# Performance work log

Hardware: AMD Instinct MI355X
Metric: run time of the kernel (lower is better)

## Reference

```python
import jax, jax.numpy as jnp
import numpy as np

N_NODES = 50000
N_EDGES = 800000
N_FEAT = 128
N_GRAPHS = 512
OUT_DIM = 128


def gcn_conv(x, W, b, src, dst, ew, n):
    """PyG GCNConv: h = x @ W; add self-loops (weight 1); symmetric norm
    D^-1/2 A D^-1/2 with edge weights; scatter-add messages src->dst; + bias."""
    h = x @ W  # [n, out]
    loop = jnp.arange(n)
    s = jnp.concatenate([src, loop])
    d = jnp.concatenate([dst, loop])
    w = jnp.concatenate([ew, jnp.ones((n,), x.dtype)])
    deg = jax.ops.segment_sum(w, d, num_segments=n)
    dinv = jnp.where(deg > 0, jax.lax.rsqrt(deg), 0.0)
    norm = dinv[s] * w * dinv[d]  # [E+n]
    out = jax.ops.segment_sum(h[s] * norm[:, None], d, num_segments=n)
    return out + b


def setup_inputs() -> dict:
    key = jax.random.key(0)
    ks = jax.random.split(key, 12)
    F = N_FEAT
    x = jax.random.normal(ks[0], (N_NODES, F), jnp.float32)
    edge_index = jax.random.randint(ks[1], (2, N_EDGES), 0, N_NODES, jnp.int64)
    edge_attr = jax.random.uniform(ks[2], (N_EDGES,), jnp.float32)
    # deterministic sorted graph assignment -> no empty graphs (avoids -inf in max pool)
    batch = (jnp.arange(N_NODES, dtype=jnp.int64) * N_GRAPHS) // N_NODES
    def lin(k, fi, fo):
        s = 1.0 / np.sqrt(fi)
        return jax.random.uniform(k, (fi, fo), jnp.float32, -s, s)
    return {
        "x": x, "edge_attr": edge_attr,
        "W1": lin(ks[3], F, F), "b1": jnp.zeros((F,), jnp.float32),
        "W2": lin(ks[4], F, 2 * F), "b2": jnp.zeros((2 * F,), jnp.float32),
        "W3": lin(ks[5], 2 * F, 4 * F), "b3": jnp.zeros((4 * F,), jnp.float32),
        "Wf1": lin(ks[6], 4 * F, 1024), "bf1": jnp.zeros((1024,), jnp.float32),
        "Wf2": lin(ks[7], 1024, OUT_DIM), "bf2": jnp.zeros((OUT_DIM,), jnp.float32),
        "edge_index": edge_index, "batch": batch,
    }


def reference(x, edge_attr, W1, b1, W2, b2, W3, b3, Wf1, bf1, Wf2, bf2,
              edge_index, batch):
    n = x.shape[0]
    src, dst = edge_index[0], edge_index[1]
    h = jax.nn.relu(gcn_conv(x, W1, b1, src, dst, edge_attr, n))
    h = jax.nn.relu(gcn_conv(h, W2, b2, src, dst, edge_attr, n))
    h = jax.nn.relu(gcn_conv(h, W3, b3, src, dst, edge_attr, n))
    # global max pool over nodes per graph
    g = jax.ops.segment_max(h, batch, num_segments=N_GRAPHS)  # [G, 4F]
    g = jax.nn.relu(g @ Wf1 + bf1)
    # dropout is identity in eval mode
    out = g @ Wf2 + bf2
    return out
```

## Files before the change

### kernel.cpp

```cpp
#include <hip/hip_runtime.h>

#define NNODES 50000
#define NEDGES 800000
#define NGRAPH 512
#define DCAP 64

typedef short bf16x8 __attribute__((ext_vector_type(8)));
typedef unsigned short u16x8 __attribute__((ext_vector_type(8)));
typedef float f32x4 __attribute__((ext_vector_type(4)));
typedef unsigned long long u64;

static __device__ __forceinline__ float b2f(unsigned short u) {
    return __uint_as_float(((unsigned)u) << 16);
}
static __device__ __forceinline__ unsigned short f2b(float f) {
    unsigned u = __float_as_uint(f);
    unsigned r = (u + 0x7fffu + ((u >> 16) & 1u)) >> 16;
    return (unsigned short)r;
}

static __device__ __forceinline__ void accum8(float (&acc)[8], float c, uint4 v) {
    unsigned w[4] = {v.x, v.y, v.z, v.w};
    #pragma unroll
    for (int i = 0; i < 4; ++i) {
        acc[2 * i]     += c * __uint_as_float(w[i] << 16);
        acc[2 * i + 1] += c * __uint_as_float(w[i] & 0xffff0000u);
    }
}

__global__ __launch_bounds__(256) void k_init(const float* __restrict__ W1, const float* __restrict__ W2,
                                              const float* __restrict__ W3, const float* __restrict__ Wf1,
                                              const float* __restrict__ Wf2,
                                              unsigned short* __restrict__ T1, unsigned short* __restrict__ T2,
                                              unsigned short* __restrict__ T3, unsigned short* __restrict__ Tf1,
                                              unsigned short* __restrict__ Tf2,
                                              u64* deg_cnt, int* gp) {
    int i = blockIdx.x * 256 + threadIdx.x;
    if (i < NNODES) deg_cnt[i] = (u64)(1u << 24);
    if (i < NGRAPH * 512) gp[i] = 0;

    const int b = blockIdx.x;
    if (b >= 204) return;
    const float* W; unsigned short* T; int K, N, t0;
    if (b < 4)        { W = W1;  T = T1;  K = 128;  N = 128;  t0 = 0;   }
    else if (b < 12)  { W = W2;  T = T2;  K = 128;  N = 256;  t0 = 4;   }
    else if (b < 44)  { W = W3;  T = T3;  K = 256;  N = 512;  t0 = 12;  }
    else if (b < 172) { W = Wf1; T = Tf1; K = 512;  N = 1024; t0 = 44;  }
    else              { W = Wf2; T = Tf2; K = 1024; N = 128;  t0 = 172; }
    const int tile = b - t0;
    const int ntn = N >> 6;
    const int k0 = (tile / ntn) * 64, n0 = (tile % ntn) * 64;
    __shared__ float sm[64][65];
    const int t = threadIdx.x;
    const int rr = t >> 6, cc = t & 63;
    #pragma unroll
    for (int r = 0; r < 16; ++r) {
        int kl = r * 4 + rr;
        sm[kl][cc] = W[(size_t)(k0 + kl) * N + n0 + cc];
    }
    __syncthreads();
    #pragma unroll
    for (int r = 0; r < 16; ++r) {
        int nl = r * 4 + rr;
        T[(size_t)(n0 + nl) * K + k0 + cc] = f2b(sm[cc][nl]);
    }
}

__global__ __launch_bounds__(256) void k_count(const int4* __restrict__ ei_s,
                                               const int4* __restrict__ ei_d,
                                               const float4* __restrict__ ew4,
                                               u64* deg_cnt,
                                               unsigned* __restrict__ edges) {
    int t = blockIdx.x * 256 + threadIdx.x;
    if (t >= NEDGES / 4) return;
    int4 ss = ei_s[t];
    int4 dd = ei_d[t];
    float4 ww = ew4[t];
    int s[4] = {ss.x, ss.y, ss.z, ss.w};
    int d[4] = {dd.x, dd.y, dd.z, dd.w};
    float w[4] = {ww.x, ww.y, ww.z, ww.w};
    int slot[4];
    #pragma unroll
    for (int u = 0; u < 4; ++u) {
        unsigned fixed = __float2uint_rn(w[u] * 16777216.0f);
        u64 old = atomicAdd(&deg_cnt[d[u]], ((u64)1 << 32) | fixed);
        slot[u] = (int)(old >> 32);
        if (slot[u] > DCAP - 1) slot[u] = DCAP - 1;
    }
    #pragma unroll
    for (int u = 0; u < 4; ++u)
        edges[((unsigned)d[u] << 6) | slot[u]] = ((unsigned)f2b(w[u]) << 16) | (unsigned)s[u];
}

__global__ void k_prep(const u64* __restrict__ deg_cnt, float* __restrict__ dinv) {
    int i = blockIdx.x * 256 + threadIdx.x;
    if (i < NNODES)
        dinv[i] = rsqrtf((float)(unsigned)(deg_cnt[i] & 0xffffffffull) * 5.9604645e-8f);
}

__global__ void k_cvt4(const float* __restrict__ X, const float* __restrict__ dinv,
                       unsigned short* __restrict__ Y, int n4) {
    int i = blockIdx.x * 256 + threadIdx.x;
    if (i < n4) {
        float4 v = ((const float4*)X)[i];
        float d = dinv[i >> 5];
        uint2 o;
        o.x = (unsigned)f2b(v.x * d) | ((unsigned)f2b(v.y * d) << 16);
        o.y = (unsigned)f2b(v.z * d) | ((unsigned)f2b(v.w * d) << 16);
        ((uint2*)Y)[i] = o;
    }
}

template <int F>
__global__ __launch_bounds__(256) void k_aggregate(const unsigned short* __restrict__ X,
                                                   const u64* __restrict__ deg_cnt,
                                                   const unsigned* __restrict__ edges,
                                                   const float* __restrict__ dinv,
                                                   unsigned short* __restrict__ Z) {
    constexpr int LPR = F / 8;
    constexpr int GRP = 64 / LPR;
    constexpr int STEP = GRP * 2;
    const int wave = threadIdx.x >> 6, lane = threadIdx.x & 63;
    const int node = blockIdx.x * 4 + wave;
    if (node >= NNODES) return;
    const int sub = lane & (LPR - 1);
    const int grp = lane / LPR;
    const int fo = sub * 8;
    const unsigned short* Xf = X + fo;
    const float di = dinv[node];
    const int cnt = (int)(deg_cnt[node] >> 32);
    const unsigned* erow = edges + ((unsigned)node << 6);

    const uint4 selfv = *(const uint4*)(Xf + (size_t)node * F);

    float acc[8] = {};

    const int e0 = grp;
    const int nb = (cnt + STEP - 1) / STEP;

    unsigned pa0 = 0, pb0 = 0, pa1 = 0, pb1 = 0;
    uint4 va0 = {}, vb0 = {};
    if (nb > 0) {
        int ea = e0, eb = e0 + GRP;
        pa0 = (ea < cnt) ? erow[ea] : 0u;
        pb0 = (eb < cnt) ? erow[eb] : 0u;
        va0 = *(const uint4*)(Xf + (size_t)(pa0 & 0xffffu) * F);
        vb0 = *(const uint4*)(Xf + (size_t)(pb0 & 0xffffu) * F);
        if (nb > 1) {
            int ea1 = e0 + STEP, eb1 = ea1 + GRP;
            pa1 = (ea1 < cnt) ? erow[ea1] : 0u;
            pb1 = (eb1 < cnt) ? erow[eb1] : 0u;
        }
    }
    for (int p = 0; p < nb; ++p) {
        uint4 va1 = {}, vb1 = {};
        unsigned pa2 = 0, pb2 = 0;
        if (p + 1 < nb) {
            va1 = *(const uint4*)(Xf + (size_t)(pa1 & 0xffffu) * F);
            vb1 = *(const uint4*)(Xf + (size_t)(pb1 & 0xffffu) * F);
            if (p + 2 < nb) {
                int ea = e0 + (p + 2) * STEP, eb = ea + GRP;
                pa2 = (ea < cnt) ? erow[ea] : 0u;
                pb2 = (eb < cnt) ? erow[eb] : 0u;
            }
        }
        accum8(acc, b2f((unsigned short)(pa0 >> 16)), va0);
        accum8(acc, b2f((unsigned short)(pb0 >> 16)), vb0);
        pa0 = pa1; pb0 = pb1; va0 = va1; vb0 = vb1;
        pa1 = pa2; pb1 = pb2;
    }

    #pragma unroll
    for (int j = 0; j < 8; ++j) {
        if constexpr (GRP == 4) acc[j] += __shfl_xor(acc[j], 16, 64);
        acc[j] += __shfl_xor(acc[j], 32, 64);
    }

    if (grp == 0) {
        unsigned w[4] = {selfv.x, selfv.y, selfv.z, selfv.w};
        unsigned o[4];
        #pragma unroll
        for (int i = 0; i < 4; ++i) {
            float s0 = __uint_as_float(w[i] << 16);
            float s1 = __uint_as_float(w[i] & 0xffff0000u);
            unsigned short c0 = f2b(di * (acc[2 * i] + s0));
            unsigned short c1 = f2b(di * (acc[2 * i + 1] + s1));
            o[i] = (unsigned)c0 | ((unsigned)c1 << 16);
        }
        uint4 ov; ov.x = o[0]; ov.y = o[1]; ov.z = o[2]; ov.w = o[3];
        *(uint4*)(Z + (size_t)node * F + fo) = ov;
    }
}

template <int CMODE, int AFP>
__global__ __launch_bounds__(256) void k_gemm_mfma(const void* __restrict__ Av,
                                                   const unsigned short* __restrict__ WT,
                                                   const float* __restrict__ bias,
                                                   void* __restrict__ Cv,
                                                   const int* __restrict__ batch,
                                                   int* __restrict__ gp,
                                                   const float* __restrict__ rscale,
                                                   int M, int N, int K) {
    constexpr int LDK = 40;
    __shared__ unsigned short As[64 * LDK];
    __shared__ unsigned short Bs[128 * LDK];
    const int tid = threadIdx.x;
    const int m0 = blockIdx.y * 64, n0 = blockIdx.x * 128;
    const int wave = tid >> 6, lane = tid & 63;
    const int wm = (wave >> 1) * 32;
    const int wn = (wave & 1) * 64;
    const int quad = lane >> 4, mrow = lane & 15;

    const int ar = tid >> 2;
    const int ak = (tid & 3) * 8;
    const bool arow_ok = (m0 + ar) < M;
    const size_t aoff = (size_t)(m0 + ar) * K + ak;
    const unsigned short* Bg0 = WT + (size_t)(n0 + ar) * K + ak;
    const unsigned short* Bg1 = WT + (size_t)(n0 + ar + 64) * K + ak;

    f32x4 acc[2][4] = {};

    for (int k0 = 0; k0 < K; k0 += 32) {
        u16x8 av = {};
        if (arow_ok) {
            if constexpr (AFP) {
                const float* Af = (const float*)Av + aoff + k0;
                float4 f0 = *(const float4*)Af;
                float4 f1 = *(const float4*)(Af + 4);
                av[0] = (short)f2b(f0.x); av[1] = (short)f2b(f0.y);
                av[2] = (short)f2b(f0.z); av[3] = (short)f2b(f0.w);
                av[4] = (short)f2b(f1.x); av[5] = (short)f2b(f1.y);
                av[6] = (short)f2b(f1.z); av[7] = (short)f2b(f1.w);
            } else {
                av = *(const u16x8*)((const unsigned short*)Av + aoff + k0);
            }
        }
        u16x8 bv0 = *(const u16x8*)(Bg0 + k0);
        u16x8 bv1 = *(const u16x8*)(Bg1 + k0);
        *(u16x8*)&As[ar * LDK + ak] = av;
        *(u16x8*)&Bs[ar * LDK + ak] = bv0;
        *(u16x8*)&Bs[(ar + 64) * LDK + ak] = bv1;
        __syncthreads();
        bf16x8 af[2], bf[4];
        #pragma unroll
        for (int mt = 0; mt < 2; ++mt)
            af[mt] = *(const bf16x8*)&As[(wm + mt * 16 + mrow) * LDK + quad * 8];
        #pragma unroll
        for (int nt = 0; nt < 4; ++nt)
            bf[nt] = *(const bf16x8*)&Bs[(wn + nt * 16 + mrow) * LDK + quad * 8];
        #pragma unroll
        for (int mt = 0; mt < 2; ++mt)
            #pragma unroll
            for (int nt = 0; nt < 4; ++nt)
                acc[mt][nt] = __builtin_amdgcn_mfma_f32_16x16x32_bf16(af[mt], bf[nt], acc[mt][nt], 0, 0, 0);
        __syncthreads();
    }

    float bn[4];
    #pragma unroll
    for (int nt = 0; nt < 4; ++nt) bn[nt] = bias[n0 + wn + nt * 16 + mrow];

    if constexpr (CMODE == 0) {
        unsigned short* C = (unsigned short*)Cv;
        #pragma unroll
        for (int mt = 0; mt < 2; ++mt) {
            #pragma unroll
            for (int r = 0; r < 4; ++r) {
                int row = m0 + wm + mt * 16 + quad * 4 + r;
                if (row < M) {
                    float rs = rscale ? rscale[row] : 1.0f;
                    #pragma unroll
                    for (int nt = 0; nt < 4; ++nt) {
                        float v = fmaxf(acc[mt][nt][r] + bn[nt], 0.f) * rs;
                        C[(size_t)row * N + n0 + wn + nt * 16 + mrow] = f2b(v);
                    }
                }
            }
        }
    } else if constexpr (CMODE == 1) {
        float* C = (float*)Cv;
        #pragma unroll
        for (int mt = 0; mt < 2; ++mt) {
            #pragma unroll
            for (int r = 0; r < 4; ++r) {
                int row = m0 + wm + mt * 16 + quad * 4 + r;
                if (row < M) {
                    #pragma unroll
                    for (int nt = 0; nt < 4; ++nt)
                        C[(size_t)row * N + n0 + wn + nt * 16 + mrow] = acc[mt][nt][r] + bn[nt];
                }
            }
        }
    } else {
        __shared__ float pools[2][2][128];
        const int g0 = batch[m0];
        int last = m0 + 63; if (last >= M) last = M - 1;
        const int gl = batch[last];
        int  gid[8];
        bool rok[8];
        #pragma unroll
        for (int mt = 0; mt < 2; ++mt)
            #pragma unroll
            for (int r = 0; r < 4; ++r) {
                int row = m0 + wm + mt * 16 + quad * 4 + r;
                rok[mt * 4 + r] = row < M;
                gid[mt * 4 + r] = (row < M) ? batch[row] : -1;
            }
        #pragma unroll
        for (int nt = 0; nt < 4; ++nt) {
            float v0 = 0.f, v1 = 0.f;
            #pragma unroll
            for (int mt = 0; mt < 2; ++mt)
                #pragma unroll
                for (int r = 0; r < 4; ++r) {
                    if (rok[mt * 4 + r]) {
                        float v = fmaxf(acc[mt][nt][r] + bn[nt], 0.f);
                        if (gid[mt * 4 + r] == g0) v0 = fmaxf(v0, v);
                        else v1 = fmaxf(v1, v);
                    }
                }
            v0 = fmaxf(v0, __shfl_xor(v0, 16, 64));
            v0 = fmaxf(v0, __shfl_xor(v0, 32, 64));
            v1 = fmaxf(v1, __shfl_xor(v1, 16, 64));
            v1 = fmaxf(v1, __shfl_xor(v1, 32, 64));
            if (quad == 0) {
                int c = wn + nt * 16 + mrow;
                pools[wm >> 5][0][c] = v0;
                pools[wm >> 5][1][c] = v1;
            }
        }
        __syncthreads();
        int c = tid & 127, gi = tid >> 7;
        float v = fmaxf(pools[0][gi][c], pools[1][gi][c]);
        int g = gi ? gl : g0;
        if (gi == 0 || gl != g0)
            atomicMax(&gp[(size_t)g * N + n0 + c], __float_as_int(v));
    }
}

extern "C" void kernel_launch(void* const* d_in, const int* in_sizes, int n_in,
                              void* d_out, int out_size, void* d_ws, size_t ws_size,
                              hipStream_t stream) {
    const float* x   = (const float*)d_in[0];
    const float* ew  = (const float*)d_in[1];
    const float* W1  = (const float*)d_in[2];
    const float* b1  = (const float*)d_in[3];
    const float* W2  = (const float*)d_in[4];
    const float* b2  = (const float*)d_in[5];
    const float* W3  = (const float*)d_in[6];
    const float* b3  = (const float*)d_in[7];
    const float* Wf1 = (const float*)d_in[8];
    const float* bf1 = (const float*)d_in[9];
    const float* Wf2 = (const float*)d_in[10];
    const float* bf2 = (const float*)d_in[11];
    const int* ei    = (const int*)d_in[12];
    const int* batch = (const int*)d_in[13];
    float* out = (float*)d_out;
    (void)in_sizes; (void)n_in; (void)out_size; (void)ws_size;

    char* p = (char*)d_ws;
    auto alloc = [&](size_t bytes) -> char* {
        char* r = p;
        p += (bytes + 255) & ~(size_t)255;
        return r;
    };
    const int nbN = (NNODES + 255) / 256;
    u64*   deg_cnt = (u64*)alloc((size_t)NNODES * 8);
    float* dinv   = (float*)alloc((size_t)NNODES * 4);
    unsigned* edges = (unsigned*)alloc((size_t)NNODES * DCAP * 4);
    int*   gp     = (int*)  alloc((size_t)NGRAPH * 512 * 4);
    unsigned short* f1   = (unsigned short*)alloc((size_t)NGRAPH * 1024 * 2);
    unsigned short* wt1  = (unsigned short*)alloc((size_t)128 * 128 * 2);
    unsigned short* wt2  = (unsigned short*)alloc((size_t)256 * 128 * 2);
    unsigned short* wt3  = (unsigned short*)alloc((size_t)512 * 256 * 2);
    unsigned short* wtf1 = (unsigned short*)alloc((size_t)1024 * 512 * 2);
    unsigned short* wtf2 = (unsigned short*)alloc((size_t)128 * 1024 * 2);
    unsigned short* bufA = (unsigned short*)alloc((size_t)NNODES * 256 * 2);
    unsigned short* bufB = (unsigned short*)alloc((size_t)NNODES * 256 * 2);
    unsigned short* x16  = bufB;

    const int MB = (NNODES + 63) / 64;
    const int AGG = (NNODES + 3) / 4;

    k_init<<<1024, 256, 0, stream>>>(W1, W2, W3, Wf1, Wf2,
                                     wt1, wt2, wt3, wtf1, wtf2, deg_cnt, gp);
    k_count<<<(NEDGES / 4 + 255) / 256, 256, 0, stream>>>(
        (const int4*)ei, (const int4*)(ei + NEDGES), (const float4*)ew, deg_cnt, edges);
    k_prep<<<nbN, 256, 0, stream>>>(deg_cnt, dinv);
    k_cvt4<<<(NNODES * 32 + 255) / 256, 256, 0, stream>>>(x, dinv, x16, NNODES * 32);

    k_aggregate<128><<<AGG, 256, 0, stream>>>(x16, deg_cnt, edges, dinv, bufA);
    k_gemm_mfma<0, 0><<<dim3(1, MB), 256, 0, stream>>>(bufA, wt1, b1, bufB, batch, nullptr, dinv, NNODES, 128, 128);
    k_aggregate<128><<<AGG, 256, 0, stream>>>(bufB, deg_cnt, edges, dinv, bufA);
    k_gemm_mfma<0, 0><<<dim3(2, MB), 256, 0, stream>>>(bufA, wt2, b2, bufB, batch, nullptr, dinv, NNODES, 256, 128);
    k_aggregate<256><<<AGG, 256, 0, stream>>>(bufB, deg_cnt, edges, dinv, bufA);
    k_gemm_mfma<2, 0><<<dim3(4, MB), 256, 0, stream>>>(bufA, wt3, b3, nullptr, batch, gp, nullptr, NNODES, 512, 256);

    k_gemm_mfma<0, 1><<<dim3(8, NGRAPH / 64), 256, 0, stream>>>(gp, wtf1, bf1, f1, batch, nullptr, nullptr, NGRAPH, 1024, 512);
    k_gemm_mfma<1, 0><<<dim3(1, NGRAPH / 64), 256, 0, stream>>>(f1, wtf2, bf2, out, batch, nullptr, nullptr, NGRAPH, 128, 1024);
}
```

Measured before the change: 364.6 us.

## Add 128x128 MFMA GEMM with direct global-to-LDS loads and XCD-aware block remap

Adds a new k_gemm128 kernel for the three node-level GEMMs. It uses 128x128 tiles with 4x4 MFMA accumulators per wave, loads tiles straight from global memory into LDS with global_load_lds, and remaps block IDs so neighbouring tiles land on the same XCD. The larger tile raises operand reuse and the direct LDS loads drop the register staging step. The pool epilogue now does atomics per wave instead of reducing through shared memory first, which roughly doubles the atomic count. Buffers are padded to NPAD so the unguarded loads of the last tile stay in bounds, though those padded rows are never initialised.

```diff
diff --git a/kernel.cpp b/kernel.cpp
--- a/kernel.cpp
+++ b/kernel.cpp
@@ -1,6 +1,7 @@
 #include <hip/hip_runtime.h>
 
 #define NNODES 50000
+#define NPAD   50048
 #define NEDGES 800000
 #define NGRAPH 512
 #define DCAP 64
@@ -9,6 +10,10 @@
 typedef unsigned short u16x8 __attribute__((ext_vector_type(8)));
 typedef float f32x4 __attribute__((ext_vector_type(4)));
 typedef unsigned long long u64;
+
+#define GLOAD16(g, l)                                                                 \
+    __builtin_amdgcn_global_load_lds((const __attribute__((address_space(1))) unsigned*)(g), \
+                                     (__attribute__((address_space(3))) unsigned*)(l), 16, 0, 0)
 
 static __device__ __forceinline__ float b2f(unsigned short u) {
     return __uint_as_float(((unsigned)u) << 16);
@@ -192,14 +197,130 @@
     }
 }
 
+template <int CMODE>
+__global__ __launch_bounds__(256) void k_gemm128(const unsigned short* __restrict__ A,
+                                                 const unsigned short* __restrict__ WT,
+                                                 const float* __restrict__ bias,
+                                                 unsigned short* __restrict__ C,
+                                                 const int* __restrict__ batch,
+                                                 int* __restrict__ gp,
+                                                 const float* __restrict__ rscale,
+                                                 int M, int N, int K) {
+    __shared__ unsigned short As[128 * 32];
+    __shared__ unsigned short Bs[128 * 32];
+    const int tid = threadIdx.x;
+
+    const int nwg = gridDim.x * gridDim.y;
+    const int f = blockIdx.y * gridDim.x + blockIdx.x;
+    const int q = nwg >> 3, r = nwg & 7;
+    const int xcd = f & 7, idx = f >> 3;
+    const int w = (xcd < r) ? xcd * (q + 1) + idx : r * (q + 1) + (xcd - r) * q + idx;
+    const int m0 = (w / gridDim.x) * 128;
+    const int n0 = (w % gridDim.x) * 128;
+
+    const int wave = tid >> 6, lane = tid & 63;
+    const int wm = (wave >> 1) * 64, wn = (wave & 1) * 64;
+    const int quad = lane >> 4, mrow = lane & 15;
+
+    const int sr = tid >> 2;
+    const int sc = (tid & 3) * 8;
+    const unsigned short* Ag0 = A + (size_t)(m0 + sr) * K + sc;
+    const unsigned short* Ag1 = A + (size_t)(m0 + 64 + sr) * K + sc;
+    const unsigned short* Bg0 = WT + (size_t)(n0 + sr) * K + sc;
+    const unsigned short* Bg1 = WT + (size_t)(n0 + 64 + sr) * K + sc;
+    unsigned short* Ad0 = &As[sr * 32 + sc];
+    unsigned short* Ad1 = &As[(64 + sr) * 32 + sc];
+    unsigned short* Bd0 = &Bs[sr * 32 + sc];
+    unsigned short* Bd1 = &Bs[(64 + sr) * 32 + sc];
+
+    f32x4 acc[4][4] = {};
+
+    for (int k0 = 0; k0 < K; k0 += 32) {
+        GLOAD16(Ag0 + k0, Ad0);
+        GLOAD16(Ag1 + k0, Ad1);
+        GLOAD16(Bg0 + k0, Bd0);
+        GLOAD16(Bg1 + k0, Bd1);
+        __syncthreads();
+        bf16x8 af[4], bf[4];
+        #pragma unroll
+        for (int mt = 0; mt < 4; ++mt)
+            af[mt] = *(const bf16x8*)&As[(wm + mt * 16 + mrow) * 32 + quad * 8];
+        #pragma unroll
+        for (int nt = 0; nt < 4; ++nt)
+            bf[nt] = *(const bf16x8*)&Bs[(wn + nt * 16 + mrow) * 32 + quad * 8];
+        #pragma unroll
+        for (int mt = 0; mt < 4; ++mt)
+            #pragma unroll
+            for (int nt = 0; nt < 4; ++nt)
+                acc[mt][nt] = __builtin_amdgcn_mfma_f32_16x16x32_bf16(af[mt], bf[nt], acc[mt][nt], 0, 0, 0);
+        __syncthreads();
+    }
+
+    float bn[4];
+    #pragma unroll
+    for (int nt = 0; nt < 4; ++nt) bn[nt] = bias[n0 + wn + nt * 16 + mrow];
+
+    if constexpr (CMODE == 0) {
+        #pragma unroll
+        for (int mt = 0; mt < 4; ++mt) {
+            #pragma unroll
+            for (int r4 = 0; r4 < 4; ++r4) {
+                int row = m0 + wm + mt * 16 + quad * 4 + r4;
+                if (row < M) {
+                    float rs = rscale ? rscale[row] : 1.0f;
+                    #pragma unroll
+                    for (int nt = 0; nt < 4; ++nt) {
+                        float v = fmaxf(acc[mt][nt][r4] + bn[nt], 0.f) * rs;
+                        C[(size_t)row * N + n0 + wn + nt * 16 + mrow] = f2b(v);
+                    }
+                }
+            }
+        }
+    } else {
+        const int wr0 = m0 + wm;
+        int g0i = wr0 < M ? wr0 : M - 1;
+        const int g0 = batch[g0i];
+        int lastr = wr0 + 63; if (lastr >= M) lastr = M - 1;
+        const int gl = batch[lastr];
+        bool rok[16]; int gid[16];
+        #pragma unroll
+        for (int mt = 0; mt < 4; ++mt)
+            #pragma unroll
+            for (int r4 = 0; r4 < 4; ++r4) {
+                int row = wr0 + mt * 16 + quad * 4 + r4;
+                rok[mt * 4 + r4] = row < M;
+                gid[mt * 4 + r4] = (row < M) ? batch[row] : -1;
+            }
+        #pragma unroll
+        for (int nt = 0; nt < 4; ++nt) {
+            float v0 = 0.f, v1 = 0.f;
+            #pragma unroll
+            for (int mt = 0; mt < 4; ++mt)
+                #pragma unroll
+                for (int r4 = 0; r4 < 4; ++r4)
+                    if (rok[mt * 4 + r4]) {
+                        float v = fmaxf(acc[mt][nt][r4] + bn[nt], 0.f);
+                        if (gid[mt * 4 + r4] == g0) v0 = fmaxf(v0, v);
+                        else v1 = fmaxf(v1, v);
+                    }
+            v0 = fmaxf(v0, __shfl_xor(v0, 16, 64));
+            v0 = fmaxf(v0, __shfl_xor(v0, 32, 64));
+            v1 = fmaxf(v1, __shfl_xor(v1, 16, 64));
+            v1 = fmaxf(v1, __shfl_xor(v1, 32, 64));
+            if (quad == 0) {
+                int c = n0 + wn + nt * 16 + mrow;
+                atomicMax(&gp[(size_t)g0 * N + c], __float_as_int(v0));
+                if (gl != g0) atomicMax(&gp[(size_t)gl * N + c], __float_as_int(v1));
+            }
+        }
+    }
+}
+
 template <int CMODE, int AFP>
 __global__ __launch_bounds__(256) void k_gemm_mfma(const void* __restrict__ Av,
                                                    const unsigned short* __restrict__ WT,
                                                    const float* __restrict__ bias,
                                                    void* __restrict__ Cv,
-                                                   const int* __restrict__ batch,
-                                                   int* __restrict__ gp,
-                                                   const float* __restrict__ rscale,
                                                    int M, int N, int K) {
     constexpr int LDK = 40;
     __shared__ unsigned short As[64 * LDK];
@@ -268,16 +389,15 @@
             for (int r = 0; r < 4; ++r) {
                 int row = m0 + wm + mt * 16 + quad * 4 + r;
                 if (row < M) {
-                    float rs = rscale ? rscale[row] : 1.0f;
                     #pragma unroll
                     for (int nt = 0; nt < 4; ++nt) {
-                        float v = fmaxf(acc[mt][nt][r] + bn[nt], 0.f) * rs;
+                        float v = fmaxf(acc[mt][nt][r] + bn[nt], 0.f);
                         C[(size_t)row * N + n0 + wn + nt * 16 + mrow] = f2b(v);
                     }
                 }
             }
         }
-    } else if constexpr (CMODE == 1) {
+    } else {
         float* C = (float*)Cv;
         #pragma unroll
         for (int mt = 0; mt < 2; ++mt) {
@@ -291,50 +411,6 @@
                 }
             }
         }
-    } else {
-        __shared__ float pools[2][2][128];
-        const int g0 = batch[m0];
-        int last = m0 + 63; if (last >= M) last = M - 1;
-        const int gl = batch[last];
-        int  gid[8];
-        bool rok[8];
-        #pragma unroll
-        for (int mt = 0; mt < 2; ++mt)
-            #pragma unroll
-            for (int r = 0; r < 4; ++r) {
-                int row = m0 + wm + mt * 16 + quad * 4 + r;
-                rok[mt * 4 + r] = row < M;
-                gid[mt * 4 + r] = (row < M) ? batch[row] : -1;
-            }
-        #pragma unroll
-        for (int nt = 0; nt < 4; ++nt) {
-            float v0 = 0.f, v1 = 0.f;
-            #pragma unroll
-            for (int mt = 0; mt < 2; ++mt)
-                #pragma unroll
-                for (int r = 0; r < 4; ++r) {
-                    if (rok[mt * 4 + r]) {
-                        float v = fmaxf(acc[mt][nt][r] + bn[nt], 0.f);
-                        if (gid[mt * 4 + r] == g0) v0 = fmaxf(v0, v);
-                        else v1 = fmaxf(v1, v);
-                    }
-                }
-            v0 = fmaxf(v0, __shfl_xor(v0, 16, 64));
-            v0 = fmaxf(v0, __shfl_xor(v0, 32, 64));
-            v1 = fmaxf(v1, __shfl_xor(v1, 16, 64));
-            v1 = fmaxf(v1, __shfl_xor(v1, 32, 64));
-            if (quad == 0) {
-                int c = wn + nt * 16 + mrow;
-                pools[wm >> 5][0][c] = v0;
-                pools[wm >> 5][1][c] = v1;
-            }
-        }
-        __syncthreads();
-        int c = tid & 127, gi = tid >> 7;
-        float v = fmaxf(pools[0][gi][c], pools[1][gi][c]);
-        int g = gi ? gl : g0;
-        if (gi == 0 || gl != g0)
-            atomicMax(&gp[(size_t)g * N + n0 + c], __float_as_int(v));
     }
 }
 
@@ -375,11 +451,11 @@
     unsigned short* wt3  = (unsigned short*)alloc((size_t)512 * 256 * 2);
     unsigned short* wtf1 = (unsigned short*)alloc((size_t)1024 * 512 * 2);
     unsigned short* wtf2 = (unsigned short*)alloc((size_t)128 * 1024 * 2);
-    unsigned short* bufA = (unsigned short*)alloc((size_t)NNODES * 256 * 2);
-    unsigned short* bufB = (unsigned short*)alloc((size_t)NNODES * 256 * 2);
+    unsigned short* bufA = (unsigned short*)alloc((size_t)NPAD * 256 * 2);
+    unsigned short* bufB = (unsigned short*)alloc((size_t)NPAD * 256 * 2);
     unsigned short* x16  = bufB;
 
-    const int MB = (NNODES + 63) / 64;
+    const int MB128 = (NNODES + 127) / 128;
     const int AGG = (NNODES + 3) / 4;
 
     k_init<<<1024, 256, 0, stream>>>(W1, W2, W3, Wf1, Wf2,
@@ -390,12 +466,12 @@
     k_cvt4<<<(NNODES * 32 + 255) / 256, 256, 0, stream>>>(x, dinv, x16, NNODES * 32);
 
     k_aggregate<128><<<AGG, 256, 0, stream>>>(x16, deg_cnt, edges, dinv, bufA);
-    k_gemm_mfma<0, 0><<<dim3(1, MB), 256, 0, stream>>>(bufA, wt1, b1, bufB, batch, nullptr, dinv, NNODES, 128, 128);
+    k_gemm128<0><<<dim3(1, MB128), 256, 0, stream>>>(bufA, wt1, b1, bufB, nullptr, nullptr, dinv, NNODES, 128, 128);
     k_aggregate<128><<<AGG, 256, 0, stream>>>(bufB, deg_cnt, edges, dinv, bufA);
-    k_gemm_mfma<0, 0><<<dim3(2, MB), 256, 0, stream>>>(bufA, wt2, b2, bufB, batch, nullptr, dinv, NNODES, 256, 128);
+    k_gemm128<0><<<dim3(2, MB128), 256, 0, stream>>>(bufA, wt2, b2, bufB, nullptr, nullptr, dinv, NNODES, 256, 128);
     k_aggregate<256><<<AGG, 256, 0, stream>>>(bufB, deg_cnt, edges, dinv, bufA);
-    k_gemm_mfma<2, 0><<<dim3(4, MB), 256, 0, stream>>>(bufA, wt3, b3, nullptr, batch, gp, nullptr, NNODES, 512, 256);
-
-    k_gemm_mfma<0, 1><<<dim3(8, NGRAPH / 64), 256, 0, stream>>>(gp, wtf1, bf1, f1, batch, nullptr, nullptr, NGRAPH, 1024, 512);
-    k_gemm_mfma<1, 0><<<dim3(1, NGRAPH / 64), 256, 0, stream>>>(f1, wtf2, bf2, out, batch, nullptr, nullptr, NGRAPH, 128, 1024);
-}
+    k_gemm128<2><<<dim3(4, MB128), 256, 0, stream>>>(bufA, wt3, b3, nullptr, batch, gp, nullptr, NNODES, 512, 256);
+
+    k_gemm_mfma<0, 1><<<dim3(8, NGRAPH / 64), 256, 0, stream>>>(gp, wtf1, bf1, f1, NGRAPH, 1024, 512);
+    k_gemm_mfma<1, 0><<<dim3(1, NGRAPH / 64), 256, 0, stream>>>(f1, wtf2, bf2, out, NGRAPH, 128, 1024);
+}
```

After: 368.4 us. Within noise of the previous version (+1.1%).
